# Kernel tuning notes

Hardware: AMD Instinct MI355X
Metric: run time of the kernel (lower is better)

## Reference

```python
import jax, jax.numpy as jnp
import numpy as np
import math

D_MODEL = 512
N_HEADS = 8
D_K = D_MODEL // N_HEADS
B, N = 2, 2048


def setup_inputs() -> dict:
    key = jax.random.key(0)
    ks = jax.random.split(key, 13)
    s = 1.0 / math.sqrt(D_MODEL)
    inp = {
        "x": jax.random.normal(ks[0], (B, N, D_MODEL), dtype=jnp.float32),
        "D": jax.random.uniform(ks[1], (B, N, N), dtype=jnp.float32),
        "A": jax.random.uniform(ks[2], (B, N, N), dtype=jnp.float32),
        "Wq": jax.random.normal(ks[3], (D_MODEL, D_MODEL), dtype=jnp.float32) * s,
        "bq": jnp.zeros((D_MODEL,), dtype=jnp.float32),
        "Wk": jax.random.normal(ks[4], (D_MODEL, D_MODEL), dtype=jnp.float32) * s,
        "bk": jnp.zeros((D_MODEL,), dtype=jnp.float32),
        "Wv": jax.random.normal(ks[5], (D_MODEL, D_MODEL), dtype=jnp.float32) * s,
        "bv": jnp.zeros((D_MODEL,), dtype=jnp.float32),
        "Wo": jax.random.normal(ks[6], (D_MODEL, D_MODEL), dtype=jnp.float32) * s,
        "bo": jnp.zeros((D_MODEL,), dtype=jnp.float32),
        # learned per-head bias scalars; init nonzero so biases matter numerically
        "w_d": jax.random.normal(ks[7], (1, N_HEADS, 1, 1), dtype=jnp.float32) * 0.1,
        "w_a": jax.random.normal(ks[8], (1, N_HEADS, 1, 1), dtype=jnp.float32) * 0.1,
    }
    return inp


def reference(x, D, A, Wq, bq, Wk, bk, Wv, bv, Wo, bo, w_d, w_a):
    b, n, _ = x.shape
    # project and split heads: (B, H, N, d_k)
    def heads(W, bias):
        return (x @ W.T + bias).reshape(b, n, N_HEADS, D_K).transpose(0, 2, 1, 3)
    q = heads(Wq, bq)
    k = heads(Wk, bk)
    v = heads(Wv, bv)
    scale = 1.0 / math.sqrt(D_K)
    # (B, H, N, N) scores with learned-scalar-weighted tree biases
    scores = jnp.einsum("bhqd,bhkd->bhqk", q, k) * scale
    scores = scores + w_d * D[:, None, :, :] + w_a * A[:, None, :, :]
    attn = jax.nn.softmax(scores, axis=-1)
    out = jnp.einsum("bhqk,bhkd->bhqd", attn, v)
    out = out.transpose(0, 2, 1, 3).reshape(b, n, D_MODEL)
    return out @ Wo.T + bo
```

## Files before the change

### kernel.cpp

```cpp
#include <hip/hip_runtime.h>
#include <hip/hip_bf16.h>
#include <math.h>

typedef unsigned short ushort_t;
typedef unsigned int   uint_t;
typedef __attribute__((ext_vector_type(8))) short  bf16x8;
typedef __attribute__((ext_vector_type(4))) float  f32x4;
typedef __attribute__((ext_vector_type(4))) int    int4v;
typedef __attribute__((ext_vector_type(2))) int    i32x2;
typedef __attribute__((ext_vector_type(4))) short  s16x4;

#define MFMA16(a, b, c) __builtin_amdgcn_mfma_f32_16x16x32_bf16((a), (b), (c), 0, 0, 0)

static constexpr int BATCH = 2;
static constexpr int SEQ   = 2048;
static constexpr int DMODEL = 512;
static constexpr int NHEADS = 8;
static constexpr int DK    = 64;
static constexpr int MROWS = BATCH * SEQ;
static constexpr int XE = MROWS * DMODEL;
static constexpr int WE = DMODEL * DMODEL;
static constexpr int NQKV = 3 * DMODEL;
static constexpr int NSPLIT = 4;
static constexpr int KB_PER = (SEQ / 64) / NSPLIT;

static constexpr float QSCALE_L2E = 0.18033688011112043f;
static constexpr float L2E = 1.4426950408889634f;

__device__ __forceinline__ ushort_t f2bf(float f) {
  unsigned int u = __builtin_bit_cast(unsigned int, f);
  u = (u + 0x7FFFu + ((u >> 16) & 1u)) >> 16;
  return (ushort_t)u;
}

__device__ __forceinline__ float fexp2(float x) {
  float r;
  asm("v_exp_f32 %0, %1" : "=v"(r) : "v"(x));
  return r;
}

__device__ __forceinline__ int cvt_pk_bf16(float a, float b) {
  int r;
  asm("v_cvt_pk_bf16_f32 %0, %1, %2" : "=v"(r) : "v"(a), "v"(b));
  return r;
}

__device__ __forceinline__ float rowmax16(float x) {
  int t;
  t = __builtin_amdgcn_mov_dpp(__builtin_bit_cast(int, x), 0xB1, 0xF, 0xF, true);
  x = fmaxf(x, __builtin_bit_cast(float, t));
  t = __builtin_amdgcn_mov_dpp(__builtin_bit_cast(int, x), 0x4E, 0xF, 0xF, true);
  x = fmaxf(x, __builtin_bit_cast(float, t));
  t = __builtin_amdgcn_mov_dpp(__builtin_bit_cast(int, x), 0x141, 0xF, 0xF, true);
  x = fmaxf(x, __builtin_bit_cast(float, t));
  t = __builtin_amdgcn_mov_dpp(__builtin_bit_cast(int, x), 0x140, 0xF, 0xF, true);
  x = fmaxf(x, __builtin_bit_cast(float, t));
  return x;
}

__device__ __forceinline__ void async16(const ushort_t* g, ushort_t* l) {
  __builtin_amdgcn_global_load_lds(
      (const __attribute__((address_space(1))) unsigned int*)g,
      (__attribute__((address_space(3))) unsigned int*)l, 16, 0, 0);
}

static constexpr int CONV_BLOCKS = (XE + 4 * WE) / 1024;
static constexpr int PACK_BLOCKS = (BATCH * SEQ * SEQ) / 1024;

__global__ __launch_bounds__(256) void convert_pack_kernel(
    const float* __restrict__ x,  const float* __restrict__ wq,
    const float* __restrict__ wk, const float* __restrict__ wv,
    const float* __restrict__ wo,
    const float* __restrict__ bq, const float* __restrict__ bk,
    const float* __restrict__ bv,
    const float* __restrict__ Dm, const float* __restrict__ Am,
    ushort_t* __restrict__ dst, float* __restrict__ bqkv,
    uint_t* __restrict__ DAb) {
  const int bid = blockIdx.x;
  if (bid == CONV_BLOCKS) {
    for (int i = threadIdx.x; i < NQKV; i += 256) {
      bqkv[i] = (i < 512) ? bq[i] * QSCALE_L2E
              : (i < 1024) ? bk[i - 512] : bv[i - 1024];
    }
    return;
  }
  if (bid > CONV_BLOCKS) {
    int e = ((bid - CONV_BLOCKS - 1) * 256 + threadIdx.x) * 4;
    float4 d = *reinterpret_cast<const float4*>(&Dm[e]);
    float4 a = *reinterpret_cast<const float4*>(&Am[e]);
    int4v v;
    v[0] = (int)((uint_t)f2bf(d.x) | ((uint_t)f2bf(a.x) << 16));
    v[1] = (int)((uint_t)f2bf(d.y) | ((uint_t)f2bf(a.y) << 16));
    v[2] = (int)((uint_t)f2bf(d.z) | ((uint_t)f2bf(a.z) << 16));
    v[3] = (int)((uint_t)f2bf(d.w) | ((uint_t)f2bf(a.w) << 16));
    *reinterpret_cast<int4v*>(&DAb[e]) = v;
    return;
  }
  int e = (bid * 256 + threadIdx.x) * 4;
  const float* src;
  int off;
  float qs = 1.0f;
  if (e < XE)                { src = x;  off = e; }
  else if (e < XE + WE)      { src = wq; off = e - XE; qs = QSCALE_L2E; }
  else if (e < XE + 2 * WE)  { src = wk; off = e - XE - WE; }
  else if (e < XE + 3 * WE)  { src = wv; off = e - XE - 2 * WE; }
  else                       { src = wo; off = e - XE - 3 * WE; }
  float4 f = *reinterpret_cast<const float4*>(&src[off]);
  s16x4 v;
  v[0] = (short)f2bf(f.x * qs); v[1] = (short)f2bf(f.y * qs);
  v[2] = (short)f2bf(f.z * qs); v[3] = (short)f2bf(f.w * qs);
  *reinterpret_cast<s16x4*>(&dst[e]) = v;
}

template <bool F32OUT>
__global__ __launch_bounds__(256) void gemm_bt128x64(
    const ushort_t* __restrict__ A, const ushort_t* __restrict__ Bt,
    const float* __restrict__ bias, void* __restrict__ C,
    int N, int K) {
  __shared__ ushort_t As[128][64];
  __shared__ ushort_t Bs[64][64];
  const int tid  = threadIdx.x;
  const int wave = tid >> 6, lane = tid & 63;
  const int quad = lane >> 4, l15 = lane & 15;
  const int m0 = blockIdx.y * 128, n0 = blockIdx.x * 64;
  const int wr = (wave >> 1) * 64, wc = (wave & 1) * 32;

  f32x4 acc[4][2] = {};

  const int lrow = lane >> 3, slot = lane & 7;
  const int cswz = 8 * (slot ^ lrow);
  const ushort_t* ag = A  + (size_t)(m0 + wave * 8 + lrow) * K + cswz;
  const ushort_t* bg = Bt + (size_t)(n0 + wave * 16 + lrow) * K + cswz;
  ushort_t* la[4];
#pragma unroll
  for (int r0 = 0; r0 < 4; r0++) la[r0] = &As[r0 * 32 + wave * 8][0];
  ushort_t* lb0 = &Bs[wave * 16][0];
  ushort_t* lb1 = &Bs[wave * 16 + 8][0];

  const int swz = l15 & 7;

  for (int k0 = 0; k0 < K; k0 += 64) {
    __syncthreads();
#pragma unroll
    for (int r0 = 0; r0 < 4; r0++)
      async16(ag + k0 + (size_t)(r0 * 32) * K, la[r0]);
    async16(bg + k0, lb0);
    async16(bg + k0 + 8 * (size_t)K, lb1);
    asm volatile("s_waitcnt vmcnt(0)" ::: "memory");
    __syncthreads();
#pragma unroll
    for (int s = 0; s < 2; s++) {
      const int acol = 8 * ((s * 4 + quad) ^ swz);
      bf16x8 af[4], bfr[2];
#pragma unroll
      for (int i = 0; i < 4; i++)
        af[i] = *reinterpret_cast<const bf16x8*>(&As[wr + i * 16 + l15][acol]);
#pragma unroll
      for (int j = 0; j < 2; j++)
        bfr[j] = *reinterpret_cast<const bf16x8*>(&Bs[wc + j * 16 + l15][acol]);
#pragma unroll
      for (int i = 0; i < 4; i++)
#pragma unroll
        for (int j = 0; j < 2; j++)
          acc[i][j] = MFMA16(af[i], bfr[j], acc[i][j]);
    }
  }

#pragma unroll
  for (int j = 0; j < 2; j++) {
    const int col = n0 + wc + j * 16 + l15;
    const float bv = bias[col];
#pragma unroll
    for (int i = 0; i < 4; i++) {
#pragma unroll
      for (int rr = 0; rr < 4; rr++) {
        const int row = m0 + wr + i * 16 + quad * 4 + rr;
        const float v = acc[i][j][rr] + bv;
        if (F32OUT) reinterpret_cast<float*>(C)[(size_t)row * N + col] = v;
        else        reinterpret_cast<ushort_t*>(C)[(size_t)row * N + col] = f2bf(v);
      }
    }
  }
}

__global__ __launch_bounds__(256) void attn_kernel(
    const ushort_t* __restrict__ QKV, const uint_t* __restrict__ DA,
    const float* __restrict__ wd, const float* __restrict__ wa,
    float* __restrict__ Opart, float* __restrict__ Mp, float* __restrict__ Lp) {
  const int qb = blockIdx.x, h = blockIdx.y;
  const int b = blockIdx.z / NSPLIT, split = blockIdx.z % NSPLIT;
  const int tid = threadIdx.x;
  const int wave = tid >> 6, lane = tid & 63;
  const int quad = lane >> 4, l15 = lane & 15;
  const int q0 = qb * 64;
  const float wdh = wd[h] * L2E, wah = wa[h] * L2E;

  __shared__ ushort_t Ks[64][64];
  __shared__ ushort_t Vts[64][64];
  __shared__ __align__(16) ushort_t Ps[4][16][72];

  const int qrow = q0 + wave * 16 + l15;
  bf16x8 qf[2];
#pragma unroll
  for (int s = 0; s < 2; s++)
    qf[s] = *reinterpret_cast<const bf16x8*>(
        &QKV[(size_t)(b * SEQ + qrow) * NQKV + h * DK + s * 32 + quad * 8]);

  bf16x8 ones;
#pragma unroll
  for (int j = 0; j < 8; j++) ones[j] = (short)0x3F80;

  float m_run[4], l_run[4];
  f32x4 o[4] = {};
#pragma unroll
  for (int rr = 0; rr < 4; rr++) { m_run[rr] = -INFINITY; l_run[rr] = 0.f; }

  const int lrow = lane >> 3, slot = lane & 7;
  const ushort_t* kg = QKV + (size_t)(b * SEQ + wave * 16 + lrow) * NQKV +
                       512 + h * DK + 8 * (slot ^ lrow);
  ushort_t* lk0 = &Ks[wave * 16][0];
  ushort_t* lk1 = &Ks[wave * 16 + 8][0];

  const int u  = tid >> 3;
  const int c7 = tid & 7;
  const int sc = c7 * 8;
  const int kv = ((u & 3) << 4) | (u >> 2);
  const ushort_t* vg = QKV + (size_t)(b * SEQ + kv) * NQKV + 1024 + h * DK + sc;
  const int col0 = (u & 7) + 8 * ((u >> 3) ^ c7);
  const int col1 = (u & 7) + 8 * (((u >> 3) + 4) ^ c7);

  const int swz = l15 & 7;
  const uint_t* DArow = DA + (size_t)b * SEQ * SEQ;

  for (int kbi = 0; kbi < KB_PER; kbi++) {
    const int k0 = (split * KB_PER + kbi) * 64;
    __syncthreads();
    async16(kg + (size_t)k0 * NQKV, lk0);
    async16(kg + (size_t)(k0 + 8) * NQKV, lk1);
    bf16x8 v0 = *reinterpret_cast<const bf16x8*>(vg + (size_t)k0 * NQKV);
    bf16x8 v1 = *reinterpret_cast<const bf16x8*>(vg + (size_t)(k0 + 8) * NQKV);
#pragma unroll
    for (int j = 0; j < 8; j++) {
      Vts[sc + j][col0] = (ushort_t)v0[j];
      Vts[sc + j][col1] = (ushort_t)v1[j];
    }
    asm volatile("s_waitcnt vmcnt(0)" ::: "memory");
    __syncthreads();

    uint_t da[4][4];
#pragma unroll
    for (int t = 0; t < 4; t++) {
      const int kk = k0 + t * 16 + l15;
#pragma unroll
      for (int rr = 0; rr < 4; rr++) {
        const int qg = q0 + wave * 16 + quad * 4 + rr;
        da[t][rr] = DArow[(size_t)qg * SEQ + kk];
      }
    }

    f32x4 sacc[4];
#pragma unroll
    for (int t = 0; t < 4; t++) {
      bf16x8 kf0 = *reinterpret_cast<const bf16x8*>(&Ks[t * 16 + l15][8 * (quad ^ swz)]);
      bf16x8 kf1 = *reinterpret_cast<const bf16x8*>(&Ks[t * 16 + l15][8 * ((4 + quad) ^ swz)]);
      f32x4 z = {};
      z = MFMA16(qf[0], kf0, z);
      sacc[t] = MFMA16(qf[1], kf1, z);
    }

    float sv[4][4];
    float mx[4] = {-INFINITY, -INFINITY, -INFINITY, -INFINITY};
#pragma unroll
    for (int t = 0; t < 4; t++) {
#pragma unroll
      for (int rr = 0; rr < 4; rr++) {
        const float fd = __builtin_bit_cast(float, da[t][rr] << 16);
        const float fa = __builtin_bit_cast(float, da[t][rr] & 0xFFFF0000u);
        float s = fmaf(wdh, fd, fmaf(wah, fa, sacc[t][rr]));
        sv[t][rr] = s;
        mx[rr] = fmaxf(mx[rr], s);
      }
    }
#pragma unroll
    for (int rr = 0; rr < 4; rr++) mx[rr] = rowmax16(mx[rr]);

    bool grow = false;
#pragma unroll
    for (int rr = 0; rr < 4; rr++) grow |= (mx[rr] > m_run[rr] + 11.5f);
    if (__ballot(grow)) {
      float alpha[4];
#pragma unroll
      for (int rr = 0; rr < 4; rr++) {
        const float mn = fmaxf(m_run[rr], mx[rr]);
        alpha[rr] = fexp2(m_run[rr] - mn);
        m_run[rr] = mn;
        l_run[rr] *= alpha[rr];
      }
#pragma unroll
      for (int dt = 0; dt < 4; dt++)
#pragma unroll
        for (int rr = 0; rr < 4; rr++) o[dt][rr] *= alpha[rr];
    }

#pragma unroll
    for (int rr = 0; rr < 4; rr++) {
      const float m = m_run[rr];
      i32x2 w;
      w[0] = cvt_pk_bf16(fexp2(sv[0][rr] - m), fexp2(sv[1][rr] - m));
      w[1] = cvt_pk_bf16(fexp2(sv[2][rr] - m), fexp2(sv[3][rr] - m));
      *reinterpret_cast<i32x2*>(&Ps[wave][quad * 4 + rr][l15 * 4]) = w;
    }

    asm volatile("s_waitcnt lgkmcnt(0)" ::: "memory");

    f32x4 rsacc = {};
#pragma unroll
    for (int s2 = 0; s2 < 2; s2++) {
      bf16x8 pf = *reinterpret_cast<const bf16x8*>(&Ps[wave][l15][s2 * 32 + quad * 8]);
#pragma unroll
      for (int dt = 0; dt < 4; dt++) {
        const int vrow = dt * 16 + l15;
        const int vcb = (s2 * 4 + quad) ^ (vrow >> 3);
        bf16x8 vf = *reinterpret_cast<const bf16x8*>(&Vts[vrow][vcb * 8]);
        o[dt] = MFMA16(pf, vf, o[dt]);
      }
      rsacc = MFMA16(pf, ones, rsacc);
    }
#pragma unroll
    for (int rr = 0; rr < 4; rr++) l_run[rr] += rsacc[rr];
  }

  const int pidx = (((b * NHEADS + h) * 32 + qb) * NSPLIT + split);
  float* op = Opart + (size_t)pidx * 4096;
#pragma unroll
  for (int dt = 0; dt < 4; dt++) {
#pragma unroll
    for (int rr = 0; rr < 4; rr++) {
      const int row = wave * 16 + quad * 4 + rr;
      op[row * 64 + dt * 16 + l15] = o[dt][rr];
    }
  }
  if (l15 == 0) {
#pragma unroll
    for (int rr = 0; rr < 4; rr++) {
      const int row = wave * 16 + quad * 4 + rr;
      Mp[(size_t)pidx * 64 + row] = m_run[rr];
      Lp[(size_t)pidx * 64 + row] = l_run[rr];
    }
  }
}

__global__ __launch_bounds__(256) void combine_kernel(
    const float* __restrict__ Opart, const float* __restrict__ Mp,
    const float* __restrict__ Lp, ushort_t* __restrict__ AO) {
  const int qb = blockIdx.x, h = blockIdx.y, b = blockIdx.z;
  const int tid = threadIdx.x;
  const int lane = tid & 63, wq = tid >> 6;
  const int pidx0 = ((b * NHEADS + h) * 32 + qb) * NSPLIT;

  for (int r = 0; r < 16; r++) {
    const int q = wq * 16 + r;
    float m[NSPLIT], l[NSPLIT];
    float M = -INFINITY;
#pragma unroll
    for (int s = 0; s < NSPLIT; s++) {
      m[s] = Mp[(size_t)(pidx0 + s) * 64 + q];
      l[s] = Lp[(size_t)(pidx0 + s) * 64 + q];
      M = fmaxf(M, m[s]);
    }
    float L = 0.f, acc = 0.f;
#pragma unroll
    for (int s = 0; s < NSPLIT; s++) {
      const float w = fexp2(m[s] - M);
      L += l[s] * w;
      acc += Opart[(size_t)(pidx0 + s) * 4096 + q * 64 + lane] * w;
    }
    const int row = b * SEQ + qb * 64 + q;
    AO[(size_t)row * DMODEL + h * DK + lane] = f2bf(acc / L);
  }
}

extern "C" void kernel_launch(void* const* d_in, const int* in_sizes, int n_in,
                              void* d_out, int out_size, void* d_ws, size_t ws_size,
                              hipStream_t stream) {
  const float* x  = (const float*)d_in[0];
  const float* Dm = (const float*)d_in[1];
  const float* Am = (const float*)d_in[2];
  const float* Wq = (const float*)d_in[3];
  const float* bq = (const float*)d_in[4];
  const float* Wk = (const float*)d_in[5];
  const float* bk = (const float*)d_in[6];
  const float* Wv = (const float*)d_in[7];
  const float* bv = (const float*)d_in[8];
  const float* Wo = (const float*)d_in[9];
  const float* bo = (const float*)d_in[10];
  const float* wd = (const float*)d_in[11];
  const float* wa = (const float*)d_in[12];

  char* ws = (char*)d_ws;
  size_t off = 0;
  ushort_t* xb    = (ushort_t*)(ws + off); off += (size_t)XE * 2;
  ushort_t* wqkvb = (ushort_t*)(ws + off); off += (size_t)3 * WE * 2;
  ushort_t* wob   = (ushort_t*)(ws + off); off += (size_t)WE * 2;
  ushort_t* QKVb  = (ushort_t*)(ws + off); off += (size_t)MROWS * NQKV * 2;
  ushort_t* AO    = (ushort_t*)(ws + off); off += (size_t)XE * 2;
  float*    bqkv  = (float*)(ws + off);    off += (size_t)NQKV * 4;
  off = (off + 255) & ~(size_t)255;
  uint_t*   DAb   = (uint_t*)(ws + off);   off += (size_t)BATCH * SEQ * SEQ * 4;
  float*    Opart = (float*)(ws + off);    off += (size_t)512 * NSPLIT * 4096 * 4;
  float*    Mpart = (float*)(ws + off);    off += (size_t)512 * NSPLIT * 64 * 4;
  float*    Lpart = (float*)(ws + off);

  convert_pack_kernel<<<CONV_BLOCKS + 1 + PACK_BLOCKS, 256, 0, stream>>>(
      x, Wq, Wk, Wv, Wo, bq, bk, bv, Dm, Am, xb, bqkv, DAb);

  dim3 qkvgrid(NQKV / 64, MROWS / 128);
  gemm_bt128x64<false><<<qkvgrid, 256, 0, stream>>>(xb, wqkvb, bqkv, QKVb, NQKV, DMODEL);

  dim3 agrid(SEQ / 64, NHEADS, BATCH * NSPLIT);
  attn_kernel<<<agrid, 256, 0, stream>>>(QKVb, DAb, wd, wa, Opart, Mpart, Lpart);
  dim3 cgrid(SEQ / 64, NHEADS, BATCH);
  combine_kernel<<<cgrid, 256, 0, stream>>>(Opart, Mpart, Lpart, AO);

  dim3 ogrid(DMODEL / 64, MROWS / 128);
  gemm_bt128x64<true><<<ogrid, 256, 0, stream>>>(AO, wob, bo, (float*)d_out, DMODEL, DMODEL);
}
```

Before: 217.8 us.

## Remap block order for XCD locality, hoist bias loads before barrier, add MFMA priority

Both the GEMM and the attention kernel remap the linear block index so that consecutive blocks sharing data (same batch and split, or nearby GEMM tiles) land on the same XCD, which should improve L2 reuse. The attention kernel now issues the global D/A bias loads before the vmcnt wait and barrier, so their latency overlaps the K/V staging. It also raises wave priority around the MFMA sections to favour matrix issue. The remap assumes the grid is divisible by 8 and that the attention grid is exactly 32x8x8.

```diff
diff --git a/kernel.cpp b/kernel.cpp
--- a/kernel.cpp
+++ b/kernel.cpp
@@ -122,7 +122,12 @@
   const int tid  = threadIdx.x;
   const int wave = tid >> 6, lane = tid & 63;
   const int quad = lane >> 4, l15 = lane & 15;
-  const int m0 = blockIdx.y * 128, n0 = blockIdx.x * 64;
+
+  const int nb  = blockIdx.x + blockIdx.y * gridDim.x;
+  const int tot = gridDim.x * gridDim.y;
+  const int w   = (nb & 7) * (tot >> 3) + (nb >> 3);
+  const int bx  = w % gridDim.x, by = w / gridDim.x;
+  const int m0 = by * 128, n0 = bx * 64;
   const int wr = (wave >> 1) * 64, wc = (wave & 1) * 32;
 
   f32x4 acc[4][2] = {};
@@ -187,8 +192,12 @@
     const ushort_t* __restrict__ QKV, const uint_t* __restrict__ DA,
     const float* __restrict__ wd, const float* __restrict__ wa,
     float* __restrict__ Opart, float* __restrict__ Mp, float* __restrict__ Lp) {
-  const int qb = blockIdx.x, h = blockIdx.y;
-  const int b = blockIdx.z / NSPLIT, split = blockIdx.z % NSPLIT;
+  const int n = blockIdx.x + (blockIdx.y << 5) + (blockIdx.z << 8);
+  const int w = ((n & 7) << 8) | (n >> 3);
+  const int h = w & 7;
+  const int qb = (w >> 3) & 31;
+  const int z = w >> 8;
+  const int b = z >> 2, split = z & 3;
   const int tid = threadIdx.x;
   const int wave = tid >> 6, lane = tid & 63;
   const int quad = lane >> 4, l15 = lane & 15;
@@ -244,8 +253,6 @@
       Vts[sc + j][col0] = (ushort_t)v0[j];
       Vts[sc + j][col1] = (ushort_t)v1[j];
     }
-    asm volatile("s_waitcnt vmcnt(0)" ::: "memory");
-    __syncthreads();
 
     uint_t da[4][4];
 #pragma unroll
@@ -258,15 +265,20 @@
       }
     }
 
+    asm volatile("s_waitcnt vmcnt(0)" ::: "memory");
+    __syncthreads();
+
     f32x4 sacc[4];
+    __builtin_amdgcn_s_setprio(1);
 #pragma unroll
     for (int t = 0; t < 4; t++) {
       bf16x8 kf0 = *reinterpret_cast<const bf16x8*>(&Ks[t * 16 + l15][8 * (quad ^ swz)]);
       bf16x8 kf1 = *reinterpret_cast<const bf16x8*>(&Ks[t * 16 + l15][8 * ((4 + quad) ^ swz)]);
-      f32x4 z = {};
-      z = MFMA16(qf[0], kf0, z);
-      sacc[t] = MFMA16(qf[1], kf1, z);
-    }
+      f32x4 z2 = {};
+      z2 = MFMA16(qf[0], kf0, z2);
+      sacc[t] = MFMA16(qf[1], kf1, z2);
+    }
+    __builtin_amdgcn_s_setprio(0);
 
     float sv[4][4];
     float mx[4] = {-INFINITY, -INFINITY, -INFINITY, -INFINITY};
@@ -305,15 +317,16 @@
 #pragma unroll
     for (int rr = 0; rr < 4; rr++) {
       const float m = m_run[rr];
-      i32x2 w;
-      w[0] = cvt_pk_bf16(fexp2(sv[0][rr] - m), fexp2(sv[1][rr] - m));
-      w[1] = cvt_pk_bf16(fexp2(sv[2][rr] - m), fexp2(sv[3][rr] - m));
-      *reinterpret_cast<i32x2*>(&Ps[wave][quad * 4 + rr][l15 * 4]) = w;
+      i32x2 wv2;
+      wv2[0] = cvt_pk_bf16(fexp2(sv[0][rr] - m), fexp2(sv[1][rr] - m));
+      wv2[1] = cvt_pk_bf16(fexp2(sv[2][rr] - m), fexp2(sv[3][rr] - m));
+      *reinterpret_cast<i32x2*>(&Ps[wave][quad * 4 + rr][l15 * 4]) = wv2;
     }
 
     asm volatile("s_waitcnt lgkmcnt(0)" ::: "memory");
 
     f32x4 rsacc = {};
+    __builtin_amdgcn_s_setprio(1);
 #pragma unroll
     for (int s2 = 0; s2 < 2; s2++) {
       bf16x8 pf = *reinterpret_cast<const bf16x8*>(&Ps[wave][l15][s2 * 32 + quad * 8]);
@@ -326,6 +339,7 @@
       }
       rsacc = MFMA16(pf, ones, rsacc);
     }
+    __builtin_amdgcn_s_setprio(0);
 #pragma unroll
     for (int rr = 0; rr < 4; rr++) l_run[rr] += rsacc[rr];
   }
```

New measurement: 211.9 us. 1.03x faster.
